# Performance work log

Hardware: AMD Instinct MI355X
Metric: run time of the kernel (lower is better)

The kernel has to match this reference:

```python
import jax, jax.numpy as jnp
import numpy as np

D_MODEL = 2048
NUM_EXPERTS = 128
TOP_K = 8
NORM_P = 2.0  # normalize_expert_weights


def setup_inputs() -> dict:
    key = jax.random.key(0)
    k1, k2 = jax.random.split(key)
    x = jax.random.normal(k1, (4, 4096, D_MODEL), dtype=jnp.float32)
    # router weight ~ trunc_normal(std=0.02); plain normal*0.02 is fine for a numeric baseline
    weight = jax.random.normal(k2, (NUM_EXPERTS, D_MODEL), dtype=jnp.float32) * 0.02
    score_bias = jnp.zeros((NUM_EXPERTS,), dtype=jnp.float32)
    return {"x": x, "weight": weight, "score_bias": score_bias}


def reference(x, weight, score_bias):
    # Flatten tokens: (B, S, D) -> (N, D); router always runs in fp32 (x.float())
    B, S, D = x.shape
    xf = x.reshape(B * S, D).astype(jnp.float32)
    # get_expert_logits: F.linear(x, weight.view(E, D)) -> (N, E)
    logits = jnp.einsum("nd,ed->ne", xf, weight.astype(jnp.float32))
    # softmax gating
    scores = jax.nn.softmax(logits, axis=-1)
    # bias-adjusted top-k (bias only affects selection, not the returned weights)
    biased = scores + score_bias[None, :]
    _, expert_indices = jax.lax.top_k(biased, TOP_K)          # (N, top_k)
    expert_weights = jnp.take_along_axis(scores, expert_indices, axis=-1)
    # normalize_expert_weights = 2.0 -> divide by L2 norm across top_k
    norm = jnp.linalg.norm(expert_weights, ord=NORM_P, axis=-1, keepdims=True)
    expert_weights = expert_weights / norm
    return expert_weights, expert_indices
```

## Files before the change

### kernel.cpp

```cpp
#include <hip/hip_runtime.h>
#include <hip/hip_bf16.h>
#include <math.h>


#define NE     128
#define TOKT   128
#define KC     32
#define KS     4
#define DMODEL 2048
#define DSLICE (DMODEL / KS)

typedef __attribute__((ext_vector_type(8))) short short8;
typedef __attribute__((ext_vector_type(4))) float f32x4;

union S8 { short s[8]; short8 v; };

__device__ __forceinline__ void split3(float f, S8& hi, S8& mi, S8& lo, int j) {
  const unsigned u0 = __float_as_uint(f);
  const float hif = __uint_as_float(u0 & 0xFFFF0000u);
  const float r1 = f - hif;
  const unsigned u1 = __float_as_uint(r1);
  const float mif = __uint_as_float(u1 & 0xFFFF0000u);
  const float r2 = r1 - mif;
  hi.s[j] = (short)(u0 >> 16);
  mi.s[j] = (short)(u1 >> 16);
  lo.s[j] = (short)(__float_as_uint(r2) >> 16);
}

__global__ __launch_bounds__(256) void logits_mfma(
    const float* __restrict__ x, const float* __restrict__ w,
    float* __restrict__ part, int N) {
  __shared__ short xs[3][TOKT][KC];
  __shared__ short wsm[3][NE][KC];

  const int tid  = threadIdx.x;
  const int wave = tid >> 6;
  const int lane = tid & 63;
  const int wm = wave >> 1;
  const int wn = wave & 1;
  const int quad = lane >> 4;
  const int l16  = lane & 15;
  const size_t tokBase = (size_t)blockIdx.x * TOKT;
  const int d0 = blockIdx.y * DSLICE;

  const int r = tid >> 1;
  const int h = tid & 1;

  f32x4 acc[4][4];
#pragma unroll
  for (int i = 0; i < 4; ++i)
#pragma unroll
    for (int j = 0; j < 4; ++j) acc[i][j] = (f32x4)(0.f);

  for (int kc = 0; kc < DSLICE; kc += KC) {
    __syncthreads();
    {
      const float* gx = x + (tokBase + r) * DMODEL + d0 + kc + h * 16;
      const float* gw = w + (size_t)r * DMODEL + d0 + kc + h * 16;
#pragma unroll
      for (int run = 0; run < 2; ++run) {
        const float4 a0 = *(const float4*)(gx + run * 8);
        const float4 a1 = *(const float4*)(gx + run * 8 + 4);
        S8 hi, mi, lo;
        split3(a0.x, hi, mi, lo, 0); split3(a0.y, hi, mi, lo, 1);
        split3(a0.z, hi, mi, lo, 2); split3(a0.w, hi, mi, lo, 3);
        split3(a1.x, hi, mi, lo, 4); split3(a1.y, hi, mi, lo, 5);
        split3(a1.z, hi, mi, lo, 6); split3(a1.w, hi, mi, lo, 7);
        const int kk = h * 16 + run * 8;
        *(short8*)&xs[0][r][kk] = hi.v;
        *(short8*)&xs[1][r][kk] = mi.v;
        *(short8*)&xs[2][r][kk] = lo.v;
        const float4 b0 = *(const float4*)(gw + run * 8);
        const float4 b1 = *(const float4*)(gw + run * 8 + 4);
        split3(b0.x, hi, mi, lo, 0); split3(b0.y, hi, mi, lo, 1);
        split3(b0.z, hi, mi, lo, 2); split3(b0.w, hi, mi, lo, 3);
        split3(b1.x, hi, mi, lo, 4); split3(b1.y, hi, mi, lo, 5);
        split3(b1.z, hi, mi, lo, 6); split3(b1.w, hi, mi, lo, 7);
        *(short8*)&wsm[0][r][kk] = hi.v;
        *(short8*)&wsm[1][r][kk] = mi.v;
        *(short8*)&wsm[2][r][kk] = lo.v;
      }
    }
    __syncthreads();

    short8 af[4][3];
#pragma unroll
    for (int mt = 0; mt < 4; ++mt)
#pragma unroll
      for (int p = 0; p < 3; ++p)
        af[mt][p] = *(const short8*)&xs[p][wm * 64 + mt * 16 + l16][quad * 8];

#pragma unroll
    for (int nt = 0; nt < 4; ++nt) {
      short8 bf[3];
#pragma unroll
      for (int p = 0; p < 3; ++p)
        bf[p] = *(const short8*)&wsm[p][wn * 64 + nt * 16 + l16][quad * 8];
#pragma unroll
      for (int mt = 0; mt < 4; ++mt) {
        f32x4 c = acc[mt][nt];
        c = __builtin_amdgcn_mfma_f32_16x16x32_bf16(af[mt][0], bf[0], c, 0, 0, 0);
        c = __builtin_amdgcn_mfma_f32_16x16x32_bf16(af[mt][0], bf[1], c, 0, 0, 0);
        c = __builtin_amdgcn_mfma_f32_16x16x32_bf16(af[mt][1], bf[0], c, 0, 0, 0);
        c = __builtin_amdgcn_mfma_f32_16x16x32_bf16(af[mt][0], bf[2], c, 0, 0, 0);
        c = __builtin_amdgcn_mfma_f32_16x16x32_bf16(af[mt][2], bf[0], c, 0, 0, 0);
        c = __builtin_amdgcn_mfma_f32_16x16x32_bf16(af[mt][1], bf[1], c, 0, 0, 0);
        acc[mt][nt] = c;
      }
    }
  }

#pragma unroll
  for (int mt = 0; mt < 4; ++mt)
#pragma unroll
    for (int nt = 0; nt < 4; ++nt) {
      const int ex = wn * 64 + nt * 16 + l16;
#pragma unroll
      for (int reg = 0; reg < 4; ++reg) {
        const size_t tok = tokBase + wm * 64 + mt * 16 + quad * 4 + reg;
        part[((size_t)blockIdx.y * N + tok) * NE + ex] = acc[mt][nt][reg];
      }
    }
}

__global__ __launch_bounds__(256) void router_topk(
    const float* __restrict__ part, const float* __restrict__ bias,
    float* __restrict__ outW, float* __restrict__ outI, int ks, int N) {
  const int wave = threadIdx.x >> 6;
  const int lane = threadIdx.x & 63;
  const int token = blockIdx.x * 4 + wave;
  if (token >= N) return;

  float l0 = 0.f, l1 = 0.f;
  for (int k = 0; k < ks; ++k) {
    const float* p = part + ((size_t)k * N + token) * NE;
    l0 += p[lane];
    l1 += p[lane + 64];
  }

  float m = fmaxf(l0, l1);
#pragma unroll
  for (int off = 1; off < 64; off <<= 1) m = fmaxf(m, __shfl_xor(m, off));
  const float ev0 = __expf(l0 - m);
  const float ev1 = __expf(l1 - m);
  float zs = ev0 + ev1;
#pragma unroll
  for (int off = 1; off < 64; off <<= 1) zs += __shfl_xor(zs, off);
  const float s0 = ev0 / zs;
  const float s1 = ev1 / zs;

  float b0 = s0 + bias[lane];
  float b1 = s1 + bias[lane + 64];

  float myv = 0.f;
  int myi = 0;
  float ss = 0.f;
#pragma unroll
  for (int rnd = 0; rnd < 8; ++rnd) {
    float key; int idx;
    if (b0 >= b1) { key = b0; idx = lane; }
    else          { key = b1; idx = lane + 64; }
#pragma unroll
    for (int off = 1; off < 64; off <<= 1) {
      const float k2 = __shfl_xor(key, off);
      const int   i2 = __shfl_xor(idx, off);
      if (k2 > key || (k2 == key && i2 < idx)) { key = k2; idx = i2; }
    }
    const float cand = (idx < 64) ? s0 : s1;
    const float sw = __shfl(cand, idx & 63);
    ss = fmaf(sw, sw, ss);
    if (lane == rnd) { myv = sw; myi = idx; }
    if (lane == (idx & 63)) { if (idx < 64) b0 = -INFINITY; else b1 = -INFINITY; }
  }

  const float inv = 1.f / sqrtf(ss);
  if (lane < 8) {
    outW[(size_t)token * 8 + lane] = myv * inv;
    outI[(size_t)token * 8 + lane] = (float)myi;
  }
}

extern "C" void kernel_launch(void* const* d_in, const int* in_sizes, int n_in,
                              void* d_out, int out_size, void* d_ws, size_t ws_size,
                              hipStream_t stream) {
  const float* x    = (const float*)d_in[0];
  const float* w    = (const float*)d_in[1];
  const float* bias = (const float*)d_in[2];
  float* out = (float*)d_out;

  const int N = in_sizes[0] / DMODEL;
  float* part = (float*)d_ws;

  logits_mfma<<<dim3(N / TOKT, KS), 256, 0, stream>>>(x, w, part, N);
  router_topk<<<(N + 3) / 4, 256, 0, stream>>>(part, bias, out, out + (size_t)N * 8, KS, N);
}
```

Measured before the change: 224.2 us.

## Fuse router GEMM with softmax/top-k and pre-split weights into MFMA fragment planes

Replaces the split-K logits kernel plus separate top-k kernel with a pre-pass that splits the router weight into bf16 hi/mid/lo planes laid out as MFMA fragments. A single fused kernel then streams x straight from global memory into registers with one-chunk-ahead prefetch, computes 32 tokens per block with no LDS staging, and runs softmax/top-k from shared memory. This removes the partial-logit round trip through global memory, the second kernel launch, and the per-block re-splitting of the weight. The cost is smaller tiles, so each x element is loaded into one block only while the weight fragments are re-read by every block from L2.

```diff
diff --git a/kernel.cpp b/kernel.cpp
--- a/kernel.cpp
+++ b/kernel.cpp
@@ -4,11 +4,12 @@
 
 
 #define NE     128
-#define TOKT   128
-#define KC     32
-#define KS     4
+#define TOKT   32
 #define DMODEL 2048
-#define DSLICE (DMODEL / KS)
+#define NCHUNK 64
+#define NSLICE 4
+#define CPS    16
+#define PSTRIDE 262144
 
 typedef __attribute__((ext_vector_type(8))) short short8;
 typedef __attribute__((ext_vector_type(4))) float f32x4;
@@ -27,156 +28,189 @@
   lo.s[j] = (short)(__float_as_uint(r2) >> 16);
 }
 
-__global__ __launch_bounds__(256) void logits_mfma(
-    const float* __restrict__ x, const float* __restrict__ w,
-    float* __restrict__ part, int N) {
-  __shared__ short xs[3][TOKT][KC];
-  __shared__ short wsm[3][NE][KC];
-
+__device__ __forceinline__ void split8(const float4& a0, const float4& a1,
+                                       S8& hi, S8& mi, S8& lo) {
+  split3(a0.x, hi, mi, lo, 0); split3(a0.y, hi, mi, lo, 1);
+  split3(a0.z, hi, mi, lo, 2); split3(a0.w, hi, mi, lo, 3);
+  split3(a1.x, hi, mi, lo, 4); split3(a1.y, hi, mi, lo, 5);
+  split3(a1.z, hi, mi, lo, 6); split3(a1.w, hi, mi, lo, 7);
+}
+
+__global__ void w_planes(const float* __restrict__ w, short* __restrict__ wfrag) {
+  const int c = blockIdx.x;
+  const int t = threadIdx.x;
+  const int e = t >> 1;
+  const int h = t & 1;
+  const float* gw = w + (size_t)e * DMODEL + c * 32 + h * 16;
+  const int g = e >> 4;
+#pragma unroll
+  for (int r2 = 0; r2 < 2; ++r2) {
+    const float4 a0 = *(const float4*)(gw + r2 * 8);
+    const float4 a1 = *(const float4*)(gw + r2 * 8 + 4);
+    S8 hi, mi, lo;
+    split8(a0, a1, hi, mi, lo);
+    const int quad = 2 * h + r2;
+    const int lane = quad * 16 + (e & 15);
+    short* base = wfrag + ((size_t)c * 8 + g) * 512 + lane * 8;
+    *(short8*)(base)               = hi.v;
+    *(short8*)(base + PSTRIDE)     = mi.v;
+    *(short8*)(base + 2 * PSTRIDE) = lo.v;
+  }
+}
+
+__global__ __launch_bounds__(256) void moe_router_fused(
+    const float* __restrict__ x, const short* __restrict__ wfrag,
+    const float* __restrict__ bias,
+    float* __restrict__ outW, float* __restrict__ outI, int N) {
+  __shared__ float ls[TOKT][NE + 4];
   const int tid  = threadIdx.x;
-  const int wave = tid >> 6;
+  const int wv   = tid >> 6;
   const int lane = tid & 63;
-  const int wm = wave >> 1;
-  const int wn = wave & 1;
   const int quad = lane >> 4;
   const int l16  = lane & 15;
   const size_t tokBase = (size_t)blockIdx.x * TOKT;
-  const int d0 = blockIdx.y * DSLICE;
-
-  const int r = tid >> 1;
-  const int h = tid & 1;
-
-  f32x4 acc[4][4];
-#pragma unroll
-  for (int i = 0; i < 4; ++i)
-#pragma unroll
-    for (int j = 0; j < 4; ++j) acc[i][j] = (f32x4)(0.f);
-
-  for (int kc = 0; kc < DSLICE; kc += KC) {
-    __syncthreads();
-    {
-      const float* gx = x + (tokBase + r) * DMODEL + d0 + kc + h * 16;
-      const float* gw = w + (size_t)r * DMODEL + d0 + kc + h * 16;
-#pragma unroll
-      for (int run = 0; run < 2; ++run) {
-        const float4 a0 = *(const float4*)(gx + run * 8);
-        const float4 a1 = *(const float4*)(gx + run * 8 + 4);
+
+  const float* xb = x + (tokBase + l16) * DMODEL + quad * 8;
+  const short* wb = wfrag + ((size_t)(wv * 2)) * 512 + lane * 8;
+
+  float4 px[4];
+  short8 pw[6];
+  px[0] = *(const float4*)(xb);
+  px[1] = *(const float4*)(xb + 4);
+  px[2] = *(const float4*)(xb + 16 * DMODEL);
+  px[3] = *(const float4*)(xb + 16 * DMODEL + 4);
+#pragma unroll
+  for (int nt = 0; nt < 2; ++nt)
+#pragma unroll
+    for (int p = 0; p < 3; ++p)
+      pw[nt * 3 + p] = *(const short8*)(wb + (size_t)p * PSTRIDE + nt * 512);
+
+  f32x4 logit[2][2];
+
+  for (int s = 0; s < NSLICE; ++s) {
+    f32x4 acc[2][2];
+#pragma unroll
+    for (int i = 0; i < 2; ++i)
+#pragma unroll
+      for (int j = 0; j < 2; ++j) acc[i][j] = (f32x4)(0.f);
+
+#pragma unroll 4
+    for (int j = 0; j < CPS; ++j) {
+      const int c = s * CPS + j;
+      short8 af[2][3], bf[2][3];
+      {
         S8 hi, mi, lo;
-        split3(a0.x, hi, mi, lo, 0); split3(a0.y, hi, mi, lo, 1);
-        split3(a0.z, hi, mi, lo, 2); split3(a0.w, hi, mi, lo, 3);
-        split3(a1.x, hi, mi, lo, 4); split3(a1.y, hi, mi, lo, 5);
-        split3(a1.z, hi, mi, lo, 6); split3(a1.w, hi, mi, lo, 7);
-        const int kk = h * 16 + run * 8;
-        *(short8*)&xs[0][r][kk] = hi.v;
-        *(short8*)&xs[1][r][kk] = mi.v;
-        *(short8*)&xs[2][r][kk] = lo.v;
-        const float4 b0 = *(const float4*)(gw + run * 8);
-        const float4 b1 = *(const float4*)(gw + run * 8 + 4);
-        split3(b0.x, hi, mi, lo, 0); split3(b0.y, hi, mi, lo, 1);
-        split3(b0.z, hi, mi, lo, 2); split3(b0.w, hi, mi, lo, 3);
-        split3(b1.x, hi, mi, lo, 4); split3(b1.y, hi, mi, lo, 5);
-        split3(b1.z, hi, mi, lo, 6); split3(b1.w, hi, mi, lo, 7);
-        *(short8*)&wsm[0][r][kk] = hi.v;
-        *(short8*)&wsm[1][r][kk] = mi.v;
-        *(short8*)&wsm[2][r][kk] = lo.v;
+        split8(px[0], px[1], hi, mi, lo);
+        af[0][0] = hi.v; af[0][1] = mi.v; af[0][2] = lo.v;
+        split8(px[2], px[3], hi, mi, lo);
+        af[1][0] = hi.v; af[1][1] = mi.v; af[1][2] = lo.v;
       }
-    }
-    __syncthreads();
-
-    short8 af[4][3];
-#pragma unroll
-    for (int mt = 0; mt < 4; ++mt)
-#pragma unroll
-      for (int p = 0; p < 3; ++p)
-        af[mt][p] = *(const short8*)&xs[p][wm * 64 + mt * 16 + l16][quad * 8];
-
-#pragma unroll
-    for (int nt = 0; nt < 4; ++nt) {
-      short8 bf[3];
-#pragma unroll
-      for (int p = 0; p < 3; ++p)
-        bf[p] = *(const short8*)&wsm[p][wn * 64 + nt * 16 + l16][quad * 8];
-#pragma unroll
-      for (int mt = 0; mt < 4; ++mt) {
-        f32x4 c = acc[mt][nt];
-        c = __builtin_amdgcn_mfma_f32_16x16x32_bf16(af[mt][0], bf[0], c, 0, 0, 0);
-        c = __builtin_amdgcn_mfma_f32_16x16x32_bf16(af[mt][0], bf[1], c, 0, 0, 0);
-        c = __builtin_amdgcn_mfma_f32_16x16x32_bf16(af[mt][1], bf[0], c, 0, 0, 0);
-        c = __builtin_amdgcn_mfma_f32_16x16x32_bf16(af[mt][0], bf[2], c, 0, 0, 0);
-        c = __builtin_amdgcn_mfma_f32_16x16x32_bf16(af[mt][2], bf[0], c, 0, 0, 0);
-        c = __builtin_amdgcn_mfma_f32_16x16x32_bf16(af[mt][1], bf[1], c, 0, 0, 0);
-        acc[mt][nt] = c;
+#pragma unroll
+      for (int nt = 0; nt < 2; ++nt)
+#pragma unroll
+        for (int p = 0; p < 3; ++p)
+          bf[nt][p] = pw[nt * 3 + p];
+
+      {
+        const int cn = (c + 1 < NCHUNK) ? c + 1 : c;
+        const float* xn = xb + cn * 32;
+        px[0] = *(const float4*)(xn);
+        px[1] = *(const float4*)(xn + 4);
+        px[2] = *(const float4*)(xn + 16 * DMODEL);
+        px[3] = *(const float4*)(xn + 16 * DMODEL + 4);
+#pragma unroll
+        for (int nt = 0; nt < 2; ++nt)
+#pragma unroll
+          for (int p = 0; p < 3; ++p)
+            pw[nt * 3 + p] = *(const short8*)(wb + (size_t)p * PSTRIDE
+                                              + (size_t)cn * 4096 + nt * 512);
       }
+
+#pragma unroll
+      for (int nt = 0; nt < 2; ++nt)
+#pragma unroll
+        for (int mt = 0; mt < 2; ++mt) {
+          f32x4 cc = acc[mt][nt];
+          cc = __builtin_amdgcn_mfma_f32_16x16x32_bf16(af[mt][0], bf[nt][0], cc, 0, 0, 0);
+          cc = __builtin_amdgcn_mfma_f32_16x16x32_bf16(af[mt][0], bf[nt][1], cc, 0, 0, 0);
+          cc = __builtin_amdgcn_mfma_f32_16x16x32_bf16(af[mt][1], bf[nt][0], cc, 0, 0, 0);
+          cc = __builtin_amdgcn_mfma_f32_16x16x32_bf16(af[mt][0], bf[nt][2], cc, 0, 0, 0);
+          cc = __builtin_amdgcn_mfma_f32_16x16x32_bf16(af[mt][2], bf[nt][0], cc, 0, 0, 0);
+          cc = __builtin_amdgcn_mfma_f32_16x16x32_bf16(af[mt][1], bf[nt][1], cc, 0, 0, 0);
+          acc[mt][nt] = cc;
+        }
+    }
+
+    if (s == 0) {
+#pragma unroll
+      for (int mt = 0; mt < 2; ++mt)
+#pragma unroll
+        for (int nt = 0; nt < 2; ++nt) logit[mt][nt] = acc[mt][nt];
+    } else {
+#pragma unroll
+      for (int mt = 0; mt < 2; ++mt)
+#pragma unroll
+        for (int nt = 0; nt < 2; ++nt) logit[mt][nt] += acc[mt][nt];
     }
   }
 
 #pragma unroll
-  for (int mt = 0; mt < 4; ++mt)
-#pragma unroll
-    for (int nt = 0; nt < 4; ++nt) {
-      const int ex = wn * 64 + nt * 16 + l16;
-#pragma unroll
-      for (int reg = 0; reg < 4; ++reg) {
-        const size_t tok = tokBase + wm * 64 + mt * 16 + quad * 4 + reg;
-        part[((size_t)blockIdx.y * N + tok) * NE + ex] = acc[mt][nt][reg];
+  for (int mt = 0; mt < 2; ++mt)
+#pragma unroll
+    for (int nt = 0; nt < 2; ++nt)
+#pragma unroll
+      for (int reg = 0; reg < 4; ++reg)
+        ls[mt * 16 + quad * 4 + reg][wv * 32 + nt * 16 + l16] = logit[mt][nt][reg];
+  __syncthreads();
+
+  const float badd0 = bias[lane];
+  const float badd1 = bias[lane + 64];
+#pragma unroll 1
+  for (int t = 0; t < 8; ++t) {
+    const int token = wv * 8 + t;
+    const float lg0 = ls[token][lane];
+    const float lg1 = ls[token][lane + 64];
+
+    float m = fmaxf(lg0, lg1);
+#pragma unroll
+    for (int off = 1; off < 64; off <<= 1) m = fmaxf(m, __shfl_xor(m, off));
+    const float ev0 = __expf(lg0 - m);
+    const float ev1 = __expf(lg1 - m);
+    float zs = ev0 + ev1;
+#pragma unroll
+    for (int off = 1; off < 64; off <<= 1) zs += __shfl_xor(zs, off);
+    const float s0 = ev0 / zs;
+    const float s1 = ev1 / zs;
+
+    float b0 = s0 + badd0;
+    float b1 = s1 + badd1;
+
+    float myv = 0.f;
+    int myi = 0;
+    float ss = 0.f;
+#pragma unroll
+    for (int rnd = 0; rnd < 8; ++rnd) {
+      float key; int idx;
+      if (b0 >= b1) { key = b0; idx = lane; }
+      else          { key = b1; idx = lane + 64; }
+#pragma unroll
+      for (int off = 1; off < 64; off <<= 1) {
+        const float k2 = __shfl_xor(key, off);
+        const int   i2 = __shfl_xor(idx, off);
+        if (k2 > key || (k2 == key && i2 < idx)) { key = k2; idx = i2; }
       }
-    }
-}
-
-__global__ __launch_bounds__(256) void router_topk(
-    const float* __restrict__ part, const float* __restrict__ bias,
-    float* __restrict__ outW, float* __restrict__ outI, int ks, int N) {
-  const int wave = threadIdx.x >> 6;
-  const int lane = threadIdx.x & 63;
-  const int token = blockIdx.x * 4 + wave;
-  if (token >= N) return;
-
-  float l0 = 0.f, l1 = 0.f;
-  for (int k = 0; k < ks; ++k) {
-    const float* p = part + ((size_t)k * N + token) * NE;
-    l0 += p[lane];
-    l1 += p[lane + 64];
-  }
-
-  float m = fmaxf(l0, l1);
-#pragma unroll
-  for (int off = 1; off < 64; off <<= 1) m = fmaxf(m, __shfl_xor(m, off));
-  const float ev0 = __expf(l0 - m);
-  const float ev1 = __expf(l1 - m);
-  float zs = ev0 + ev1;
-#pragma unroll
-  for (int off = 1; off < 64; off <<= 1) zs += __shfl_xor(zs, off);
-  const float s0 = ev0 / zs;
-  const float s1 = ev1 / zs;
-
-  float b0 = s0 + bias[lane];
-  float b1 = s1 + bias[lane + 64];
-
-  float myv = 0.f;
-  int myi = 0;
-  float ss = 0.f;
-#pragma unroll
-  for (int rnd = 0; rnd < 8; ++rnd) {
-    float key; int idx;
-    if (b0 >= b1) { key = b0; idx = lane; }
-    else          { key = b1; idx = lane + 64; }
-#pragma unroll
-    for (int off = 1; off < 64; off <<= 1) {
-      const float k2 = __shfl_xor(key, off);
-      const int   i2 = __shfl_xor(idx, off);
-      if (k2 > key || (k2 == key && i2 < idx)) { key = k2; idx = i2; }
-    }
-    const float cand = (idx < 64) ? s0 : s1;
-    const float sw = __shfl(cand, idx & 63);
-    ss = fmaf(sw, sw, ss);
-    if (lane == rnd) { myv = sw; myi = idx; }
-    if (lane == (idx & 63)) { if (idx < 64) b0 = -INFINITY; else b1 = -INFINITY; }
-  }
-
-  const float inv = 1.f / sqrtf(ss);
-  if (lane < 8) {
-    outW[(size_t)token * 8 + lane] = myv * inv;
-    outI[(size_t)token * 8 + lane] = (float)myi;
+      const float cand = (idx < 64) ? s0 : s1;
+      const float sw = __shfl(cand, idx & 63);
+      ss = fmaf(sw, sw, ss);
+      if (lane == rnd) { myv = sw; myi = idx; }
+      if (lane == (idx & 63)) { if (idx < 64) b0 = -INFINITY; else b1 = -INFINITY; }
+    }
+
+    const float inv = 1.f / sqrtf(ss);
+    if (lane < 8) {
+      outW[(tokBase + token) * 8 + lane] = myv * inv;
+      outI[(tokBase + token) * 8 + lane] = (float)myi;
+    }
   }
 }
 
@@ -189,8 +223,9 @@
   float* out = (float*)d_out;
 
   const int N = in_sizes[0] / DMODEL;
-  float* part = (float*)d_ws;
-
-  logits_mfma<<<dim3(N / TOKT, KS), 256, 0, stream>>>(x, w, part, N);
-  router_topk<<<(N + 3) / 4, 256, 0, stream>>>(part, bias, out, out + (size_t)N * 8, KS, N);
-}
+  short* wfrag = (short*)d_ws;
+
+  w_planes<<<NCHUNK, 256, 0, stream>>>(w, wfrag);
+  moe_router_fused<<<N / TOKT, 256, 0, stream>>>(x, wfrag, bias,
+                                                 out, out + (size_t)N * 8, N);
+}
```

Measured after the change: 297.8 us. 1.33x slower.
